# Optimization experiments

Hardware: AMD Instinct MI355X
Metric: run time of the kernel (lower is better)

## Reference

```python
import jax, jax.numpy as jnp
import numpy as np

N = 16_777_216
NUM_GRAPHS = 16_384
POS_WEIGHT = 7.0
POSITION_WEIGHT = 0.1


def setup_inputs() -> dict:
    key = jax.random.key(0)
    k1, k2, k3 = jax.random.split(key, 3)
    logits = jax.random.normal(k1, (N, 2), dtype=jnp.float32)
    labels = jax.random.randint(k2, (N,), 0, 2, dtype=jnp.int64)
    batch = jnp.sort(jax.random.randint(k3, (N,), 0, NUM_GRAPHS, dtype=jnp.int64))
    return {"logits": logits, "labels": labels, "batch": batch}


def reference(logits, labels, batch):
    # weighted cross-entropy, torch semantics: sum(w[y]*nll) / sum(w[y])
    class_weight = jnp.array([1.0, POS_WEIGHT], dtype=logits.dtype)
    logp = jax.nn.log_softmax(logits, axis=1)          # [N, 2]
    nll = -jnp.take_along_axis(logp, labels[:, None], axis=1)[:, 0]  # [N]
    w = class_weight[labels]                            # [N]
    ce = jnp.sum(w * nll) / jnp.sum(w)

    # position loss: |p1[i] - p1[i+1]| over consecutive nodes in the same
    # graph where either endpoint has label 1 (vectorized shift form of the
    # original nested per-graph loop; nodes of a graph are contiguous)
    p1 = jnp.exp(logp[:, 1])                            # softmax prob of class 1
    same_graph = batch[1:] == batch[:-1]
    pos_pair = (labels[:-1] == 1) | (labels[1:] == 1)
    mask = (same_graph & pos_pair).astype(p1.dtype)
    position_loss = jnp.sum(jnp.abs(p1[1:] - p1[:-1]) * mask)

    return ce + POSITION_WEIGHT * position_loss
```

## Files before the change

### kernel.cpp

```cpp
#include <hip/hip_runtime.h>
#include <math.h>

#define POS_WEIGHT 7.0f
#define POSITION_WEIGHT 0.1f
#define BLOCK 256
#define STEP 2048
#define STEPS 4
#define RPB (STEP * STEPS)

__device__ __forceinline__ float sigp(float d) {
    float e  = __expf(-fabsf(d));
    float rt = __builtin_amdgcn_rcpf(1.0f + e);
    return (d >= 0.0f ? 1.0f : e) * rt;
}

__device__ __forceinline__ void acc_nll(int la, float p, float& s_wnll, float& s_w) {
    float sel = la ? p : 1.0f - p;
    float w   = la ? POS_WEIGHT : 1.0f;
    s_wnll = fmaf(w, -__logf(sel), s_wnll);
    s_w += w;
}

__device__ __forceinline__ void pair_term(int la0, int ba0, float p0,
                                          int la1, int ba1, float p1, float& s_pos) {
    if (ba0 == ba1 && (la0 | la1)) s_pos += fabsf(p1 - p0);
}

__global__ __launch_bounds__(BLOCK, 4) void pos_loss_kernel(
    const float* __restrict__ logits,
    const int*   __restrict__ labels,
    const int*   __restrict__ batch,
    float4* __restrict__ partials,
    int n)
{
    __shared__ __align__(16) float Pf[STEP + 8];
    __shared__ int   Mb[2 * BLOCK];
    __shared__ float prevP;
    __shared__ int   prevM;

    const int t  = threadIdx.x;
    const long long bb = (long long)blockIdx.x * RPB;

    float s_wnll = 0.f, s_w = 0.f, s_pos = 0.f;
    float carry_p = 0.f; int carry_m = -2;

    if (t == BLOCK - 1 && bb > 0 && bb < n) {
        int i = (int)bb - 1;
        float2 lp = ((const float2*)logits)[i];
        carry_p = sigp(lp.y - lp.x);
        carry_m = (batch[i] << 1) | labels[i];
    }

    for (int s = 0; s < STEPS; ++s) {
        const long long row0l = bb + (long long)s * STEP;
        if (row0l >= n) break;
        const int row0 = (int)row0l;

        if (row0 + STEP <= n) {
            const float4* lg4 = (const float4*)logits + (row0 >> 1);
            const int4*   lb4 = (const int4*)labels + (row0 >> 2);
            const int4*   bt4 = (const int4*)batch  + (row0 >> 2);

            float4 L0 = lg4[t];
            float4 L1 = lg4[256 + t];
            float4 L2 = lg4[512 + t];
            float4 L3 = lg4[768 + t];
            int4 laA = lb4[t];
            int4 laB = lb4[256 + t];
            int4 baA = bt4[t];
            int4 baB = bt4[256 + t];

            if (t == BLOCK - 1) { prevP = carry_p; prevM = carry_m; }

            float2* P2 = (float2*)Pf;
            P2[t]       = make_float2(sigp(L0.y - L0.x), sigp(L0.w - L0.z));
            P2[256 + t] = make_float2(sigp(L1.y - L1.x), sigp(L1.w - L1.z));
            P2[512 + t] = make_float2(sigp(L2.y - L2.x), sigp(L2.w - L2.z));
            P2[768 + t] = make_float2(sigp(L3.y - L3.x), sigp(L3.w - L3.z));
            Mb[t]         = (baA.x << 1) | laA.x;
            Mb[BLOCK + t] = (baB.x << 1) | laB.x;
            __syncthreads();

            float4 pA = ((const float4*)Pf)[t];
            float4 pB = ((const float4*)Pf)[256 + t];
            float pA4 = Pf[4 * t + 4];
            float pB4 = Pf[1024 + 4 * t + 4];

            acc_nll(laA.x, pA.x, s_wnll, s_w);
            acc_nll(laA.y, pA.y, s_wnll, s_w);
            acc_nll(laA.z, pA.z, s_wnll, s_w);
            acc_nll(laA.w, pA.w, s_wnll, s_w);
            acc_nll(laB.x, pB.x, s_wnll, s_w);
            acc_nll(laB.y, pB.y, s_wnll, s_w);
            acc_nll(laB.z, pB.z, s_wnll, s_w);
            acc_nll(laB.w, pB.w, s_wnll, s_w);

            pair_term(laA.x, baA.x, pA.x, laA.y, baA.y, pA.y, s_pos);
            pair_term(laA.y, baA.y, pA.y, laA.z, baA.z, pA.z, s_pos);
            pair_term(laA.z, baA.z, pA.z, laA.w, baA.w, pA.w, s_pos);
            { int m = Mb[t + 1]; pair_term(laA.w, baA.w, pA.w, m & 1, m >> 1, pA4, s_pos); }
            pair_term(laB.x, baB.x, pB.x, laB.y, baB.y, pB.y, s_pos);
            pair_term(laB.y, baB.y, pB.y, laB.z, baB.z, pB.z, s_pos);
            pair_term(laB.z, baB.z, pB.z, laB.w, baB.w, pB.w, s_pos);
            if (t < BLOCK - 1) {
                int m = Mb[BLOCK + t + 1];
                pair_term(laB.w, baB.w, pB.w, m & 1, m >> 1, pB4, s_pos);
            }
            if (t == 0)
                pair_term(prevM & 1, prevM >> 1, prevP, laA.x, baA.x, pA.x, s_pos);
            if (t == BLOCK - 1) { carry_p = pB.w; carry_m = (baB.w << 1) | laB.w; }
            __syncthreads();
        } else {
            if (t == BLOCK - 1) { prevP = carry_p; prevM = carry_m; }
            __syncthreads();
            for (int g = 0; g < 2; ++g) {
                int rb = row0 + g * 1024 + 4 * t;
                #pragma unroll
                for (int k = 0; k < 4; ++k) {
                    int r = rb + k;
                    if (r < n) {
                        float2 lp = ((const float2*)logits)[r];
                        int la = labels[r], ba = batch[r];
                        float p = sigp(lp.y - lp.x);
                        acc_nll(la, p, s_wnll, s_w);
                        if (r + 1 < n) {
                            float2 lq = ((const float2*)logits)[r + 1];
                            pair_term(la, ba, p, labels[r + 1], batch[r + 1],
                                      sigp(lq.y - lq.x), s_pos);
                        }
                    }
                }
            }
            if (t == 0) {
                float2 lp = ((const float2*)logits)[row0];
                pair_term(prevM & 1, prevM >> 1, prevP,
                          labels[row0], batch[row0], sigp(lp.y - lp.x), s_pos);
            }
            __syncthreads();
        }
    }

    #pragma unroll
    for (int off = 32; off > 0; off >>= 1) {
        s_wnll += __shfl_down(s_wnll, off);
        s_w    += __shfl_down(s_w, off);
        s_pos  += __shfl_down(s_pos, off);
    }
    __shared__ float sa[BLOCK / 64], sb[BLOCK / 64], sc[BLOCK / 64];
    int lane = t & 63, wid = t >> 6;
    if (lane == 0) { sa[wid] = s_wnll; sb[wid] = s_w; sc[wid] = s_pos; }
    __syncthreads();
    if (t == 0) {
        float ta = 0.f, tb = 0.f, tc = 0.f;
        #pragma unroll
        for (int w = 0; w < BLOCK / 64; ++w) { ta += sa[w]; tb += sb[w]; tc += sc[w]; }
        partials[blockIdx.x] = make_float4(ta, tb, tc, 0.f);
    }
}

__global__ __launch_bounds__(256) void finalize_kernel(
    const float4* __restrict__ partials, int nb, float* __restrict__ out)
{
    float a = 0.f, b = 0.f, c = 0.f;
    for (int i = threadIdx.x; i < nb; i += 256) {
        float4 v = partials[i];
        a += v.x; b += v.y; c += v.z;
    }
    #pragma unroll
    for (int off = 32; off > 0; off >>= 1) {
        a += __shfl_down(a, off);
        b += __shfl_down(b, off);
        c += __shfl_down(c, off);
    }
    __shared__ float sa[4], sb[4], sc[4];
    int lane = threadIdx.x & 63, wid = threadIdx.x >> 6;
    if (lane == 0) { sa[wid] = a; sb[wid] = b; sc[wid] = c; }
    __syncthreads();
    if (threadIdx.x == 0) {
        float ta = 0.f, tb = 0.f, tc = 0.f;
        #pragma unroll
        for (int w = 0; w < 4; ++w) { ta += sa[w]; tb += sb[w]; tc += sc[w]; }
        out[0] = ta / tb + POSITION_WEIGHT * tc;
    }
}

extern "C" void kernel_launch(void* const* d_in, const int* in_sizes, int n_in,
                              void* d_out, int out_size, void* d_ws, size_t ws_size,
                              hipStream_t stream) {
    const float* logits = (const float*)d_in[0];
    const int*   labels = (const int*)d_in[1];
    const int*   batch  = (const int*)d_in[2];
    float* out = (float*)d_out;
    float4* partials = (float4*)d_ws;
    int n = in_sizes[1];

    int nblocks = (n + RPB - 1) / RPB;
    pos_loss_kernel<<<nblocks, BLOCK, 0, stream>>>(logits, labels, batch, partials, n);
    finalize_kernel<<<1, 256, 0, stream>>>(partials, nblocks, out);
}
```

Measured before the change: 48.14 us.

## Process one 2048-row tile per block instead of looping four tiles

Removes the per-block loop over four tiles, so each block handles a single 2048-row tile and the grid grows fourfold. The boundary element from the previous tile is now loaded directly from global memory instead of being carried between iterations, and the occupancy hint in launch bounds is dropped. This trades the serialized in-block load/compute/sync phases for more blocks in flight to hide memory latency. The cost is more partials for the single-block finalize kernel to reduce and one extra scattered load per block.

```diff
diff --git a/kernel.cpp b/kernel.cpp
--- a/kernel.cpp
+++ b/kernel.cpp
@@ -5,8 +5,6 @@
 #define POSITION_WEIGHT 0.1f
 #define BLOCK 256
 #define STEP 2048
-#define STEPS 4
-#define RPB (STEP * STEPS)
 
 __device__ __forceinline__ float sigp(float d) {
     float e  = __expf(-fabsf(d));
@@ -26,7 +24,7 @@
     if (ba0 == ba1 && (la0 | la1)) s_pos += fabsf(p1 - p0);
 }
 
-__global__ __launch_bounds__(BLOCK, 4) void pos_loss_kernel(
+__global__ __launch_bounds__(BLOCK) void pos_loss_kernel(
     const float* __restrict__ logits,
     const int*   __restrict__ labels,
     const int*   __restrict__ batch,
@@ -38,105 +36,106 @@
     __shared__ float prevP;
     __shared__ int   prevM;
 
-    const int t  = threadIdx.x;
-    const long long bb = (long long)blockIdx.x * RPB;
+    const int t    = threadIdx.x;
+    const int row0 = blockIdx.x * STEP;
 
     float s_wnll = 0.f, s_w = 0.f, s_pos = 0.f;
-    float carry_p = 0.f; int carry_m = -2;
 
-    if (t == BLOCK - 1 && bb > 0 && bb < n) {
-        int i = (int)bb - 1;
-        float2 lp = ((const float2*)logits)[i];
-        carry_p = sigp(lp.y - lp.x);
-        carry_m = (batch[i] << 1) | labels[i];
-    }
+    if (row0 + STEP <= n) {
+        const float4* lg4 = (const float4*)logits + (row0 >> 1);
+        const int4*   lb4 = (const int4*)labels + (row0 >> 2);
+        const int4*   bt4 = (const int4*)batch  + (row0 >> 2);
 
-    for (int s = 0; s < STEPS; ++s) {
-        const long long row0l = bb + (long long)s * STEP;
-        if (row0l >= n) break;
-        const int row0 = (int)row0l;
+        float4 L0 = lg4[t];
+        float4 L1 = lg4[256 + t];
+        float4 L2 = lg4[512 + t];
+        float4 L3 = lg4[768 + t];
+        int4 laA = lb4[t];
+        int4 laB = lb4[256 + t];
+        int4 baA = bt4[t];
+        int4 baB = bt4[256 + t];
 
-        if (row0 + STEP <= n) {
-            const float4* lg4 = (const float4*)logits + (row0 >> 1);
-            const int4*   lb4 = (const int4*)labels + (row0 >> 2);
-            const int4*   bt4 = (const int4*)batch  + (row0 >> 2);
+        if (t == BLOCK - 1) {
+            if (row0 > 0) {
+                int i = row0 - 1;
+                float2 lp = ((const float2*)logits)[i];
+                prevP = sigp(lp.y - lp.x);
+                prevM = (batch[i] << 1) | labels[i];
+            } else {
+                prevP = 0.f; prevM = -2;
+            }
+        }
 
-            float4 L0 = lg4[t];
-            float4 L1 = lg4[256 + t];
-            float4 L2 = lg4[512 + t];
-            float4 L3 = lg4[768 + t];
-            int4 laA = lb4[t];
-            int4 laB = lb4[256 + t];
-            int4 baA = bt4[t];
-            int4 baB = bt4[256 + t];
+        float2* P2 = (float2*)Pf;
+        P2[t]       = make_float2(sigp(L0.y - L0.x), sigp(L0.w - L0.z));
+        P2[256 + t] = make_float2(sigp(L1.y - L1.x), sigp(L1.w - L1.z));
+        P2[512 + t] = make_float2(sigp(L2.y - L2.x), sigp(L2.w - L2.z));
+        P2[768 + t] = make_float2(sigp(L3.y - L3.x), sigp(L3.w - L3.z));
+        Mb[t]         = (baA.x << 1) | laA.x;
+        Mb[BLOCK + t] = (baB.x << 1) | laB.x;
+        __syncthreads();
 
-            if (t == BLOCK - 1) { prevP = carry_p; prevM = carry_m; }
+        float4 pA = ((const float4*)Pf)[t];
+        float4 pB = ((const float4*)Pf)[256 + t];
+        float pA4 = Pf[4 * t + 4];
+        float pB4 = Pf[1024 + 4 * t + 4];
 
-            float2* P2 = (float2*)Pf;
-            P2[t]       = make_float2(sigp(L0.y - L0.x), sigp(L0.w - L0.z));
-            P2[256 + t] = make_float2(sigp(L1.y - L1.x), sigp(L1.w - L1.z));
-            P2[512 + t] = make_float2(sigp(L2.y - L2.x), sigp(L2.w - L2.z));
-            P2[768 + t] = make_float2(sigp(L3.y - L3.x), sigp(L3.w - L3.z));
-            Mb[t]         = (baA.x << 1) | laA.x;
-            Mb[BLOCK + t] = (baB.x << 1) | laB.x;
-            __syncthreads();
+        acc_nll(laA.x, pA.x, s_wnll, s_w);
+        acc_nll(laA.y, pA.y, s_wnll, s_w);
+        acc_nll(laA.z, pA.z, s_wnll, s_w);
+        acc_nll(laA.w, pA.w, s_wnll, s_w);
+        acc_nll(laB.x, pB.x, s_wnll, s_w);
+        acc_nll(laB.y, pB.y, s_wnll, s_w);
+        acc_nll(laB.z, pB.z, s_wnll, s_w);
+        acc_nll(laB.w, pB.w, s_wnll, s_w);
 
-            float4 pA = ((const float4*)Pf)[t];
-            float4 pB = ((const float4*)Pf)[256 + t];
-            float pA4 = Pf[4 * t + 4];
-            float pB4 = Pf[1024 + 4 * t + 4];
-
-            acc_nll(laA.x, pA.x, s_wnll, s_w);
-            acc_nll(laA.y, pA.y, s_wnll, s_w);
-            acc_nll(laA.z, pA.z, s_wnll, s_w);
-            acc_nll(laA.w, pA.w, s_wnll, s_w);
-            acc_nll(laB.x, pB.x, s_wnll, s_w);
-            acc_nll(laB.y, pB.y, s_wnll, s_w);
-            acc_nll(laB.z, pB.z, s_wnll, s_w);
-            acc_nll(laB.w, pB.w, s_wnll, s_w);
-
-            pair_term(laA.x, baA.x, pA.x, laA.y, baA.y, pA.y, s_pos);
-            pair_term(laA.y, baA.y, pA.y, laA.z, baA.z, pA.z, s_pos);
-            pair_term(laA.z, baA.z, pA.z, laA.w, baA.w, pA.w, s_pos);
-            { int m = Mb[t + 1]; pair_term(laA.w, baA.w, pA.w, m & 1, m >> 1, pA4, s_pos); }
-            pair_term(laB.x, baB.x, pB.x, laB.y, baB.y, pB.y, s_pos);
-            pair_term(laB.y, baB.y, pB.y, laB.z, baB.z, pB.z, s_pos);
-            pair_term(laB.z, baB.z, pB.z, laB.w, baB.w, pB.w, s_pos);
-            if (t < BLOCK - 1) {
-                int m = Mb[BLOCK + t + 1];
-                pair_term(laB.w, baB.w, pB.w, m & 1, m >> 1, pB4, s_pos);
+        pair_term(laA.x, baA.x, pA.x, laA.y, baA.y, pA.y, s_pos);
+        pair_term(laA.y, baA.y, pA.y, laA.z, baA.z, pA.z, s_pos);
+        pair_term(laA.z, baA.z, pA.z, laA.w, baA.w, pA.w, s_pos);
+        { int m = Mb[t + 1]; pair_term(laA.w, baA.w, pA.w, m & 1, m >> 1, pA4, s_pos); }
+        pair_term(laB.x, baB.x, pB.x, laB.y, baB.y, pB.y, s_pos);
+        pair_term(laB.y, baB.y, pB.y, laB.z, baB.z, pB.z, s_pos);
+        pair_term(laB.z, baB.z, pB.z, laB.w, baB.w, pB.w, s_pos);
+        if (t < BLOCK - 1) {
+            int m = Mb[BLOCK + t + 1];
+            pair_term(laB.w, baB.w, pB.w, m & 1, m >> 1, pB4, s_pos);
+        }
+        if (t == 0)
+            pair_term(prevM & 1, prevM >> 1, prevP, laA.x, baA.x, pA.x, s_pos);
+    } else if (row0 < n) {
+        if (t == BLOCK - 1) {
+            if (row0 > 0) {
+                int i = row0 - 1;
+                float2 lp = ((const float2*)logits)[i];
+                prevP = sigp(lp.y - lp.x);
+                prevM = (batch[i] << 1) | labels[i];
+            } else {
+                prevP = 0.f; prevM = -2;
             }
-            if (t == 0)
-                pair_term(prevM & 1, prevM >> 1, prevP, laA.x, baA.x, pA.x, s_pos);
-            if (t == BLOCK - 1) { carry_p = pB.w; carry_m = (baB.w << 1) | laB.w; }
-            __syncthreads();
-        } else {
-            if (t == BLOCK - 1) { prevP = carry_p; prevM = carry_m; }
-            __syncthreads();
-            for (int g = 0; g < 2; ++g) {
-                int rb = row0 + g * 1024 + 4 * t;
-                #pragma unroll
-                for (int k = 0; k < 4; ++k) {
-                    int r = rb + k;
-                    if (r < n) {
-                        float2 lp = ((const float2*)logits)[r];
-                        int la = labels[r], ba = batch[r];
-                        float p = sigp(lp.y - lp.x);
-                        acc_nll(la, p, s_wnll, s_w);
-                        if (r + 1 < n) {
-                            float2 lq = ((const float2*)logits)[r + 1];
-                            pair_term(la, ba, p, labels[r + 1], batch[r + 1],
-                                      sigp(lq.y - lq.x), s_pos);
-                        }
+        }
+        __syncthreads();
+        for (int g = 0; g < 2; ++g) {
+            int rb = row0 + g * 1024 + 4 * t;
+            #pragma unroll
+            for (int k = 0; k < 4; ++k) {
+                int r = rb + k;
+                if (r < n) {
+                    float2 lp = ((const float2*)logits)[r];
+                    int la = labels[r], ba = batch[r];
+                    float p = sigp(lp.y - lp.x);
+                    acc_nll(la, p, s_wnll, s_w);
+                    if (r + 1 < n) {
+                        float2 lq = ((const float2*)logits)[r + 1];
+                        pair_term(la, ba, p, labels[r + 1], batch[r + 1],
+                                  sigp(lq.y - lq.x), s_pos);
                     }
                 }
             }
-            if (t == 0) {
-                float2 lp = ((const float2*)logits)[row0];
-                pair_term(prevM & 1, prevM >> 1, prevP,
-                          labels[row0], batch[row0], sigp(lp.y - lp.x), s_pos);
-            }
-            __syncthreads();
+        }
+        if (t == 0) {
+            float2 lp = ((const float2*)logits)[row0];
+            pair_term(prevM & 1, prevM >> 1, prevP,
+                      labels[row0], batch[row0], sigp(lp.y - lp.x), s_pos);
         }
     }
 
@@ -194,7 +193,7 @@
     float4* partials = (float4*)d_ws;
     int n = in_sizes[1];
 
-    int nblocks = (n + RPB - 1) / RPB;
+    int nblocks = (n + STEP - 1) / STEP;
     pos_loss_kernel<<<nblocks, BLOCK, 0, stream>>>(logits, labels, batch, partials, n);
     finalize_kernel<<<1, 256, 0, stream>>>(partials, nblocks, out);
 }
```

Measured after the change: 53.63 us. 11.4% more time.

## Replace LDS staging with wavefront shuffles for neighbor pair terms

Applied to the files above, without the earlier changes.

Each thread now handles two rows per iteration through float4 logit loads and int2 label/batch loads, in a grid-stride-free loop of 16 units. Neighbour values across threads come from __shfl_down instead of a shared-memory tile with two __syncthreads per step. Lane 63 fetches its right neighbour straight from global memory. This drops the LDS round trip and block barriers, at the cost of narrower per-thread loads (int2 instead of int4) and an extra scattered global read per wavefront per iteration.

```diff
diff --git a/kernel.cpp b/kernel.cpp
--- a/kernel.cpp
+++ b/kernel.cpp
@@ -4,9 +4,7 @@
 #define POS_WEIGHT 7.0f
 #define POSITION_WEIGHT 0.1f
 #define BLOCK 256
-#define STEP 2048
-#define STEPS 4
-#define RPB (STEP * STEPS)
+#define UPT 16
 
 __device__ __forceinline__ float sigp(float d) {
     float e  = __expf(-fabsf(d));
@@ -33,110 +31,58 @@
     float4* __restrict__ partials,
     int n)
 {
-    __shared__ __align__(16) float Pf[STEP + 8];
-    __shared__ int   Mb[2 * BLOCK];
-    __shared__ float prevP;
-    __shared__ int   prevM;
-
-    const int t  = threadIdx.x;
-    const long long bb = (long long)blockIdx.x * RPB;
+    const int t    = threadIdx.x;
+    const int lane = t & 63;
+    const int NU   = n >> 1;
+    const int upb  = BLOCK * UPT;
+    const int g0   = blockIdx.x * upb;
 
     float s_wnll = 0.f, s_w = 0.f, s_pos = 0.f;
-    float carry_p = 0.f; int carry_m = -2;
 
-    if (t == BLOCK - 1 && bb > 0 && bb < n) {
-        int i = (int)bb - 1;
-        float2 lp = ((const float2*)logits)[i];
-        carry_p = sigp(lp.y - lp.x);
-        carry_m = (batch[i] << 1) | labels[i];
+    const float4* lg4 = (const float4*)logits;
+    const int2*   lb2 = (const int2*)labels;
+    const int2*   bt2 = (const int2*)batch;
+
+    #pragma unroll 4
+    for (int it = 0; it < UPT; ++it) {
+        const int g = g0 + it * BLOCK + t;
+        float p0 = 0.f, p1 = 0.f;
+        int2 la = make_int2(0, 0), ba = make_int2(-3, -3);
+
+        if (g < NU) {
+            float4 L = lg4[g];
+            la = lb2[g];
+            ba = bt2[g];
+            p0 = sigp(L.y - L.x);
+            p1 = sigp(L.w - L.z);
+            acc_nll(la.x, p0, s_wnll, s_w);
+            acc_nll(la.y, p1, s_wnll, s_w);
+            pair_term(la.x, ba.x, p0, la.y, ba.y, p1, s_pos);
+        }
+
+        float np0 = __shfl_down(p0, 1);
+        int   nla = __shfl_down(la.x, 1);
+        int   nba = __shfl_down(ba.x, 1);
+        if (lane == 63 && g + 1 < NU) {
+            float2 lp = ((const float2*)logits)[2 * g + 2];
+            np0 = sigp(lp.y - lp.x);
+            nla = labels[2 * g + 2];
+            nba = batch[2 * g + 2];
+        }
+        if (g + 1 < NU)
+            pair_term(la.y, ba.y, p1, nla, nba, np0, s_pos);
     }
 
-    for (int s = 0; s < STEPS; ++s) {
-        const long long row0l = bb + (long long)s * STEP;
-        if (row0l >= n) break;
-        const int row0 = (int)row0l;
-
-        if (row0 + STEP <= n) {
-            const float4* lg4 = (const float4*)logits + (row0 >> 1);
-            const int4*   lb4 = (const int4*)labels + (row0 >> 2);
-            const int4*   bt4 = (const int4*)batch  + (row0 >> 2);
-
-            float4 L0 = lg4[t];
-            float4 L1 = lg4[256 + t];
-            float4 L2 = lg4[512 + t];
-            float4 L3 = lg4[768 + t];
-            int4 laA = lb4[t];
-            int4 laB = lb4[256 + t];
-            int4 baA = bt4[t];
-            int4 baB = bt4[256 + t];
-
-            if (t == BLOCK - 1) { prevP = carry_p; prevM = carry_m; }
-
-            float2* P2 = (float2*)Pf;
-            P2[t]       = make_float2(sigp(L0.y - L0.x), sigp(L0.w - L0.z));
-            P2[256 + t] = make_float2(sigp(L1.y - L1.x), sigp(L1.w - L1.z));
-            P2[512 + t] = make_float2(sigp(L2.y - L2.x), sigp(L2.w - L2.z));
-            P2[768 + t] = make_float2(sigp(L3.y - L3.x), sigp(L3.w - L3.z));
-            Mb[t]         = (baA.x << 1) | laA.x;
-            Mb[BLOCK + t] = (baB.x << 1) | laB.x;
-            __syncthreads();
-
-            float4 pA = ((const float4*)Pf)[t];
-            float4 pB = ((const float4*)Pf)[256 + t];
-            float pA4 = Pf[4 * t + 4];
-            float pB4 = Pf[1024 + 4 * t + 4];
-
-            acc_nll(laA.x, pA.x, s_wnll, s_w);
-            acc_nll(laA.y, pA.y, s_wnll, s_w);
-            acc_nll(laA.z, pA.z, s_wnll, s_w);
-            acc_nll(laA.w, pA.w, s_wnll, s_w);
-            acc_nll(laB.x, pB.x, s_wnll, s_w);
-            acc_nll(laB.y, pB.y, s_wnll, s_w);
-            acc_nll(laB.z, pB.z, s_wnll, s_w);
-            acc_nll(laB.w, pB.w, s_wnll, s_w);
-
-            pair_term(laA.x, baA.x, pA.x, laA.y, baA.y, pA.y, s_pos);
-            pair_term(laA.y, baA.y, pA.y, laA.z, baA.z, pA.z, s_pos);
-            pair_term(laA.z, baA.z, pA.z, laA.w, baA.w, pA.w, s_pos);
-            { int m = Mb[t + 1]; pair_term(laA.w, baA.w, pA.w, m & 1, m >> 1, pA4, s_pos); }
-            pair_term(laB.x, baB.x, pB.x, laB.y, baB.y, pB.y, s_pos);
-            pair_term(laB.y, baB.y, pB.y, laB.z, baB.z, pB.z, s_pos);
-            pair_term(laB.z, baB.z, pB.z, laB.w, baB.w, pB.w, s_pos);
-            if (t < BLOCK - 1) {
-                int m = Mb[BLOCK + t + 1];
-                pair_term(laB.w, baB.w, pB.w, m & 1, m >> 1, pB4, s_pos);
-            }
-            if (t == 0)
-                pair_term(prevM & 1, prevM >> 1, prevP, laA.x, baA.x, pA.x, s_pos);
-            if (t == BLOCK - 1) { carry_p = pB.w; carry_m = (baB.w << 1) | laB.w; }
-            __syncthreads();
-        } else {
-            if (t == BLOCK - 1) { prevP = carry_p; prevM = carry_m; }
-            __syncthreads();
-            for (int g = 0; g < 2; ++g) {
-                int rb = row0 + g * 1024 + 4 * t;
-                #pragma unroll
-                for (int k = 0; k < 4; ++k) {
-                    int r = rb + k;
-                    if (r < n) {
-                        float2 lp = ((const float2*)logits)[r];
-                        int la = labels[r], ba = batch[r];
-                        float p = sigp(lp.y - lp.x);
-                        acc_nll(la, p, s_wnll, s_w);
-                        if (r + 1 < n) {
-                            float2 lq = ((const float2*)logits)[r + 1];
-                            pair_term(la, ba, p, labels[r + 1], batch[r + 1],
-                                      sigp(lq.y - lq.x), s_pos);
-                        }
-                    }
-                }
-            }
-            if (t == 0) {
-                float2 lp = ((const float2*)logits)[row0];
-                pair_term(prevM & 1, prevM >> 1, prevP,
-                          labels[row0], batch[row0], sigp(lp.y - lp.x), s_pos);
-            }
-            __syncthreads();
+    if ((n & 1) && blockIdx.x == 0 && t == 0) {
+        int r = n - 1;
+        float2 lp = ((const float2*)logits)[r];
+        float p = sigp(lp.y - lp.x);
+        int la1 = labels[r], ba1 = batch[r];
+        acc_nll(la1, p, s_wnll, s_w);
+        if (r > 0) {
+            float2 lq = ((const float2*)logits)[r - 1];
+            pair_term(labels[r - 1], batch[r - 1], sigp(lq.y - lq.x),
+                      la1, ba1, p, s_pos);
         }
     }
 
@@ -147,7 +93,7 @@
         s_pos  += __shfl_down(s_pos, off);
     }
     __shared__ float sa[BLOCK / 64], sb[BLOCK / 64], sc[BLOCK / 64];
-    int lane = t & 63, wid = t >> 6;
+    int wid = t >> 6;
     if (lane == 0) { sa[wid] = s_wnll; sb[wid] = s_w; sc[wid] = s_pos; }
     __syncthreads();
     if (t == 0) {
@@ -194,7 +140,9 @@
     float4* partials = (float4*)d_ws;
     int n = in_sizes[1];
 
-    int nblocks = (n + RPB - 1) / RPB;
+    int NU = n >> 1;
+    int upb = BLOCK * UPT;
+    int nblocks = (NU + upb - 1) / upb;
     pos_loss_kernel<<<nblocks, BLOCK, 0, stream>>>(logits, labels, batch, partials, n);
     finalize_kernel<<<1, 256, 0, stream>>>(partials, nblocks, out);
 }
```

Result: no change. 48.11 us (-0.1%).
